# Kernel optimization log

Hardware: AMD Instinct MI355X
Metric: run time of the kernel (lower is better)

## Reference

```python
import jax, jax.numpy as jnp
import numpy as np

N_NODES = 50000
N_EDGES = 640000
IN_FEATS = 128
OUT_FEATS = 64
K = 2  # number of sparse sum-aggregation hops


def setup_inputs() -> dict:
    key = jax.random.key(0)
    k1, k2, k3, k4, k5 = jax.random.split(key, 5)
    features = jax.random.normal(k1, (N_NODES, IN_FEATS), dtype=jnp.float32)
    src = jax.random.randint(k2, (N_EDGES,), 0, N_NODES, dtype=jnp.int64)
    dst = jax.random.randint(k3, (N_EDGES,), 0, N_NODES, dtype=jnp.int64)
    weight = jax.random.normal(k4, (IN_FEATS, OUT_FEATS), dtype=jnp.float32) * (IN_FEATS ** -0.5)
    bias = jax.random.normal(k5, (OUT_FEATS,), dtype=jnp.float32) * 0.02
    return {"features": features, "src": src, "dst": dst, "weight": weight, "bias": bias}


def reference(features, src, dst, weight, bias):
    N = features.shape[0]
    ones = jnp.ones(src.shape[0], dtype=features.dtype)
    # degrees (graph is static across hops)
    out_deg = jax.ops.segment_sum(ones, src, num_segments=N)  # out-degree of each node
    in_deg = jax.ops.segment_sum(ones, dst, num_segments=N)   # in-degree of each node
    norm_src = jax.lax.rsqrt(jnp.clip(out_deg, 1.0))[:, None]
    norm_dst = jax.lax.rsqrt(jnp.clip(in_deg, 1.0))[:, None]

    # K hops of unnormalized copy_u/sum message passing
    h = features
    for _ in range(K):
        h = jax.ops.segment_sum(h[src], dst, num_segments=N)

    # GraphConv with norm='both': D_in^{-1/2} A^T D_out^{-1/2} h W + b
    h = h * norm_src
    h = h @ weight  # in_feats > out_feats: project before aggregating
    h = jax.ops.segment_sum(h[src], dst, num_segments=N)
    h = h * norm_dst + bias
    return h
```

## Files before the change

kernel.cpp:

```cpp
#include <hip/hip_runtime.h>
#include <hip/hip_bf16.h>

#define IN_FEATS 128
#define OUT_FEATS 64
#define HB_D 128
#define HB_S 64
#define PB 256
#define MAX_WORDS 12544
#define SMEM_U32 12544
#define PROJ_NODES 256

static inline char* align_up(char* p, size_t a) {
    return (char*)(((uintptr_t)p + a - 1) & ~(uintptr_t)(a - 1));
}

__device__ __forceinline__ unsigned pack_bf16(float a, float b) {
    unsigned ua = __float_as_uint(a), ub = __float_as_uint(b);
    ua = (ua + 0x7fffu + ((ua >> 16) & 1u)) >> 16;
    ub = (ub + 0x7fffu + ((ub >> 16) & 1u)) >> 16;
    return ua | (ub << 16);
}
__device__ __forceinline__ float bf16_lo(unsigned u) { return __uint_as_float(u << 16); }
__device__ __forceinline__ float bf16_hi(unsigned u) { return __uint_as_float(u & 0xffff0000u); }

__global__ __launch_bounds__(1024)
void hist_kernel(const int* __restrict__ src, const int* __restrict__ dst,
                 unsigned* __restrict__ partial, int* __restrict__ gcounter,
                 int E, int slice_d, int slice_s, int words) {
    __shared__ unsigned h[SMEM_U32];
    int tid = (int)threadIdx.x;
    int b = (int)blockIdx.x;

    if (b == 0 && tid == 0) *gcounter = 0;

    for (int w = tid; w < words; w += 1024) h[w] = 0u;
    __syncthreads();
    const int* __restrict__ keys;
    int sb, se;
    if (b < HB_D) { keys = dst; sb = b * slice_d; se = min(sb + slice_d, E); }
    else          { keys = src; sb = (b - HB_D) * slice_s; se = min(sb + slice_s, E); }
    for (int i = sb + tid * 4; i < se; i += 1024 * 4) {
        if (i + 3 < se) {
            int4 k4 = *reinterpret_cast<const int4*>(keys + i);
            atomicAdd(&h[k4.x >> 2], 1u << ((k4.x & 3) * 8));
            atomicAdd(&h[k4.y >> 2], 1u << ((k4.y & 3) * 8));
            atomicAdd(&h[k4.z >> 2], 1u << ((k4.z & 3) * 8));
            atomicAdd(&h[k4.w >> 2], 1u << ((k4.w & 3) * 8));
        } else {
            for (int j = i; j < se; ++j) {
                int k = keys[j];
                atomicAdd(&h[k >> 2], 1u << ((k & 3) * 8));
            }
        }
    }
    __syncthreads();
    unsigned* __restrict__ outp = partial + (size_t)b * words;
    for (int w = tid; w < words; w += 1024) outp[w] = h[w];
}

__global__ __launch_bounds__(PB)
void prefix_alloc_kernel(const unsigned* __restrict__ partial, unsigned* __restrict__ pprefix,
                         int2* __restrict__ rowext, float* __restrict__ normS,
                         float* __restrict__ normD, int* __restrict__ gcounter,
                         int N, int words) {
    __shared__ int tsum[PB];
    __shared__ int s_base;
    int tid = (int)threadIdx.x;
    int w = (int)blockIdx.x * PB + tid;
    unsigned run = 0, ssum = 0;
    if (w < words) {
        for (int bb = 0; bb < HB_D; bb += 16) {
            unsigned v[16], pfx[16];
#pragma unroll
            for (int i = 0; i < 16; ++i) v[i] = partial[(size_t)(bb + i) * words + w];
#pragma unroll
            for (int i = 0; i < 16; ++i) { pfx[i] = run; run += v[i]; }
#pragma unroll
            for (int i = 0; i < 16; ++i) pprefix[(size_t)(bb + i) * words + w] = pfx[i];
        }
        for (int bb = HB_D; bb < HB_D + HB_S; bb += 16) {
            unsigned v[16];
#pragma unroll
            for (int i = 0; i < 16; ++i) v[i] = partial[(size_t)(bb + i) * words + w];
#pragma unroll
            for (int i = 0; i < 16; ++i) ssum += v[i];
        }
    }
    int c0 = (int)(run & 0xffu), c1 = (int)((run >> 8) & 0xffu);
    int c2 = (int)((run >> 16) & 0xffu), c3 = (int)(run >> 24);
    int dtot = c0 + c1 + c2 + c3;
    tsum[tid] = dtot;
    __syncthreads();
    for (int off = 1; off < PB; off <<= 1) {
        int t = (tid >= off) ? tsum[tid - off] : 0;
        __syncthreads();
        tsum[tid] += t;
        __syncthreads();
    }
    if (tid == PB - 1) s_base = atomicAdd(gcounter, tsum[PB - 1]);
    __syncthreads();
    if (w < words) {
        int excl = tsum[tid] - dtot + s_base;
        int r0 = excl, r1 = r0 + c0, r2 = r1 + c1, r3 = r2 + c2;
        int base = 4 * w;
        if (base + 3 < N) {
            int4* re = reinterpret_cast<int4*>(rowext + base);
            re[0] = make_int4(r0, r1, r1, r2);
            re[1] = make_int4(r2, r3, r3, r3 + c3);
            float4 nD = make_float4(rsqrtf(fmaxf((float)c0, 1.f)), rsqrtf(fmaxf((float)c1, 1.f)),
                                    rsqrtf(fmaxf((float)c2, 1.f)), rsqrtf(fmaxf((float)c3, 1.f)));
            int s0 = (int)(ssum & 0xffu), s1 = (int)((ssum >> 8) & 0xffu);
            int s2 = (int)((ssum >> 16) & 0xffu), s3 = (int)(ssum >> 24);
            float4 nS = make_float4(rsqrtf(fmaxf((float)s0, 1.f)), rsqrtf(fmaxf((float)s1, 1.f)),
                                    rsqrtf(fmaxf((float)s2, 1.f)), rsqrtf(fmaxf((float)s3, 1.f)));
            *reinterpret_cast<float4*>(normD + base) = nD;
            *reinterpret_cast<float4*>(normS + base) = nS;
        } else {
            int r[5] = {r0, r1, r2, r3, r3 + c3};
            int cD[4] = {c0, c1, c2, c3};
            int cS[4] = {(int)(ssum & 0xffu), (int)((ssum >> 8) & 0xffu),
                         (int)((ssum >> 16) & 0xffu), (int)(ssum >> 24)};
            for (int i = 0; i < 4 && base + i < N; ++i) {
                rowext[base + i] = make_int2(r[i], r[i + 1]);
                normD[base + i] = rsqrtf(fmaxf((float)cD[i], 1.f));
                normS[base + i] = rsqrtf(fmaxf((float)cS[i], 1.f));
            }
        }
    }
}

__global__ __launch_bounds__(1024)
void fill_proj_kernel(const int* __restrict__ src, const int* __restrict__ dst,
                      const unsigned* __restrict__ pprefix, const int2* __restrict__ rowext,
                      unsigned short* __restrict__ csr16,
                      const float* __restrict__ X, const float* __restrict__ W,
                      uint2* __restrict__ Y,
                      int N, int E, int slice_d, int words) {
    __shared__ unsigned smem[SMEM_U32];
    int tid = (int)threadIdx.x;
    int b = (int)blockIdx.x;

    if (b < HB_D) {
        const unsigned* __restrict__ pp = pprefix + (size_t)b * words;
        for (int w = tid; w < words; w += 1024) smem[w] = pp[w];
        __syncthreads();
        int sb = b * slice_d;
        int se = min(sb + slice_d, E);
        for (int i = sb + tid * 4; i < se; i += 1024 * 4) {
            if (i + 3 < se) {
                int4 d4 = *reinterpret_cast<const int4*>(dst + i);
                int4 s4 = *reinterpret_cast<const int4*>(src + i);
                int dd[4] = {d4.x, d4.y, d4.z, d4.w};
                int ss[4] = {s4.x, s4.y, s4.z, s4.w};
#pragma unroll
                for (int j = 0; j < 4; ++j) {
                    int bin = dd[j];
                    unsigned sh = (unsigned)(bin & 3) * 8u;
                    unsigned old = atomicAdd(&smem[bin >> 2], 1u << sh);
                    int off = (int)((old >> sh) & 0xffu);
                    csr16[rowext[bin].x + off] = (unsigned short)ss[j];
                }
            } else {
                for (int j = i; j < se; ++j) {
                    int bin = dst[j];
                    unsigned sh = (unsigned)(bin & 3) * 8u;
                    unsigned old = atomicAdd(&smem[bin >> 2], 1u << sh);
                    int off = (int)((old >> sh) & 0xffu);
                    csr16[rowext[bin].x + off] = (unsigned short)src[j];
                }
            }
        }
    } else {
        float* w_s = (float*)smem;
        for (int i = tid; i < IN_FEATS * OUT_FEATS / 4; i += 1024)
            reinterpret_cast<float4*>(w_s)[i] = reinterpret_cast<const float4*>(W)[i];
        __syncthreads();
        int slot = tid >> 4;
        int jj = (tid & 15) * 4;
        int n0 = (b - HB_D) * PROJ_NODES + slot * 4;
        int m0 = min(n0 + 0, N - 1), m1 = min(n0 + 1, N - 1);
        int m2 = min(n0 + 2, N - 1), m3 = min(n0 + 3, N - 1);
        const float* __restrict__ x0p = X + (size_t)m0 * IN_FEATS;
        const float* __restrict__ x1p = X + (size_t)m1 * IN_FEATS;
        const float* __restrict__ x2p = X + (size_t)m2 * IN_FEATS;
        const float* __restrict__ x3p = X + (size_t)m3 * IN_FEATS;
        float4 a0 = make_float4(0.f, 0.f, 0.f, 0.f), a1 = a0, a2 = a0, a3 = a0;
#pragma unroll 2
        for (int k = 0; k < IN_FEATS; k += 4) {
            float4 x0 = *reinterpret_cast<const float4*>(x0p + k);
            float4 x1 = *reinterpret_cast<const float4*>(x1p + k);
            float4 x2 = *reinterpret_cast<const float4*>(x2p + k);
            float4 x3 = *reinterpret_cast<const float4*>(x3p + k);
#pragma unroll
            for (int q = 0; q < 4; ++q) {
                float4 w = *reinterpret_cast<const float4*>(&w_s[(k + q) * OUT_FEATS + jj]);
                float e0 = (q == 0) ? x0.x : (q == 1) ? x0.y : (q == 2) ? x0.z : x0.w;
                float e1 = (q == 0) ? x1.x : (q == 1) ? x1.y : (q == 2) ? x1.z : x1.w;
                float e2 = (q == 0) ? x2.x : (q == 1) ? x2.y : (q == 2) ? x2.z : x2.w;
                float e3 = (q == 0) ? x3.x : (q == 1) ? x3.y : (q == 2) ? x3.z : x3.w;
                a0.x = fmaf(e0, w.x, a0.x); a0.y = fmaf(e0, w.y, a0.y);
                a0.z = fmaf(e0, w.z, a0.z); a0.w = fmaf(e0, w.w, a0.w);
                a1.x = fmaf(e1, w.x, a1.x); a1.y = fmaf(e1, w.y, a1.y);
                a1.z = fmaf(e1, w.z, a1.z); a1.w = fmaf(e1, w.w, a1.w);
                a2.x = fmaf(e2, w.x, a2.x); a2.y = fmaf(e2, w.y, a2.y);
                a2.z = fmaf(e2, w.z, a2.z); a2.w = fmaf(e2, w.w, a2.w);
                a3.x = fmaf(e3, w.x, a3.x); a3.y = fmaf(e3, w.y, a3.y);
                a3.z = fmaf(e3, w.z, a3.z); a3.w = fmaf(e3, w.w, a3.w);
            }
        }
        float4 accs[4] = {a0, a1, a2, a3};
#pragma unroll
        for (int i = 0; i < 4; ++i) {
            int node = n0 + i;
            if (node < N) {
                uint2 o;
                o.x = pack_bf16(accs[i].x, accs[i].y);
                o.y = pack_bf16(accs[i].z, accs[i].w);
                Y[(size_t)node * (OUT_FEATS / 4) + (jj >> 2)] = o;
            }
        }
    }
}

template <int EPI>
__global__ __launch_bounds__(256)
void gather_hop(const uint4* __restrict__ Yin, const int2* __restrict__ rowext,
                const unsigned short* __restrict__ csr16, void* __restrict__ Yout,
                const float* __restrict__ vec, const float* __restrict__ bias,
                int N) {
    int g = ((int)threadIdx.x >> 3) & 7;
    int ci = (int)threadIdx.x & 7;
    int wid = (int)blockIdx.x * 4 + ((int)threadIdx.x >> 6);
    int nwaves = (int)gridDim.x * 4;
    for (int n0 = wid * 8; n0 < N; n0 += nwaves * 8) {
        int node = n0 + g;
        int beg = 0, end = 0;
        if (node < N) {
            int2 be = rowext[node];
            beg = be.x; end = be.y;
        }
        float4 aA = make_float4(0.f, 0.f, 0.f, 0.f), aB = aA;
        float4 bA = aA, bB = aA;
        int k = beg;
        for (; k + 1 < end; k += 2) {
            int s0 = (int)csr16[k];
            int s1 = (int)csr16[k + 1];
            uint4 v0 = Yin[(size_t)s0 * 8 + ci];
            uint4 v1 = Yin[(size_t)s1 * 8 + ci];
            aA.x += bf16_lo(v0.x); aA.y += bf16_hi(v0.x);
            aA.z += bf16_lo(v0.y); aA.w += bf16_hi(v0.y);
            aB.x += bf16_lo(v0.z); aB.y += bf16_hi(v0.z);
            aB.z += bf16_lo(v0.w); aB.w += bf16_hi(v0.w);
            bA.x += bf16_lo(v1.x); bA.y += bf16_hi(v1.x);
            bA.z += bf16_lo(v1.y); bA.w += bf16_hi(v1.y);
            bB.x += bf16_lo(v1.z); bB.y += bf16_hi(v1.z);
            bB.z += bf16_lo(v1.w); bB.w += bf16_hi(v1.w);
        }
        if (k < end) {
            uint4 v = Yin[(size_t)csr16[k] * 8 + ci];
            aA.x += bf16_lo(v.x); aA.y += bf16_hi(v.x);
            aA.z += bf16_lo(v.y); aA.w += bf16_hi(v.y);
            aB.x += bf16_lo(v.z); aB.y += bf16_hi(v.z);
            aB.z += bf16_lo(v.w); aB.w += bf16_hi(v.w);
        }
        if (node < N) {
            aA.x += bA.x; aA.y += bA.y; aA.z += bA.z; aA.w += bA.w;
            aB.x += bB.x; aB.y += bB.y; aB.z += bB.z; aB.w += bB.w;
            if (EPI == 1) {
                float sc = vec[node];
                aA.x *= sc; aA.y *= sc; aA.z *= sc; aA.w *= sc;
                aB.x *= sc; aB.y *= sc; aB.z *= sc; aB.w *= sc;
            }
            if (EPI == 2) {
                float sc = vec[node];
                float4 b0 = *reinterpret_cast<const float4*>(bias + ci * 8);
                float4 b1 = *reinterpret_cast<const float4*>(bias + ci * 8 + 4);
                aA.x = fmaf(aA.x, sc, b0.x); aA.y = fmaf(aA.y, sc, b0.y);
                aA.z = fmaf(aA.z, sc, b0.z); aA.w = fmaf(aA.w, sc, b0.w);
                aB.x = fmaf(aB.x, sc, b1.x); aB.y = fmaf(aB.y, sc, b1.y);
                aB.z = fmaf(aB.z, sc, b1.w == b1.w ? b1.z : b1.z); aB.w = fmaf(aB.w, sc, b1.w);
                float* op = (float*)Yout + (size_t)node * OUT_FEATS + ci * 8;
                *reinterpret_cast<float4*>(op) = aA;
                *reinterpret_cast<float4*>(op + 4) = aB;
            } else {
                uint4 o;
                o.x = pack_bf16(aA.x, aA.y);
                o.y = pack_bf16(aA.z, aA.w);
                o.z = pack_bf16(aB.x, aB.y);
                o.w = pack_bf16(aB.z, aB.w);
                reinterpret_cast<uint4*>(Yout)[(size_t)node * 8 + ci] = o;
            }
        }
    }
}

extern "C" void kernel_launch(void* const* d_in, const int* in_sizes, int n_in,
                              void* d_out, int out_size, void* d_ws, size_t ws_size,
                              hipStream_t stream) {
    const float* features = (const float*)d_in[0];
    const int*   src      = (const int*)d_in[1];
    const int*   dst      = (const int*)d_in[2];
    const float* weight   = (const float*)d_in[3];
    const float* bias     = (const float*)d_in[4];

    const int N = in_sizes[0] / IN_FEATS;
    const int E = in_sizes[1];
    const int words = (N + 3) / 4;
    const int NB = (words + PB - 1) / PB;
    const int slice_d = (((E + HB_D - 1) / HB_D) + 3) & ~3;
    const int slice_s = (((E + HB_S - 1) / HB_S) + 3) & ~3;
    const int projBlocks = (N + PROJ_NODES - 1) / PROJ_NODES;

    char* p = (char*)d_ws;
    float* normS   = (float*)p;  p = align_up(p + sizeof(float) * (N + 4), 256);
    float* normD   = (float*)p;  p = align_up(p + sizeof(float) * (N + 4), 256);
    uint2* y0      = (uint2*)p;  p = align_up(p + sizeof(uint2) * (size_t)N * (OUT_FEATS / 4), 256);
    uint2* y1      = (uint2*)p;  p = align_up(p + sizeof(uint2) * (size_t)N * (OUT_FEATS / 4), 256);
    int2*  rowext  = (int2*)p;   p = align_up(p + sizeof(int2) * (N + 4), 256);
    int*   gcounter= (int*)p;    p = align_up(p + sizeof(int) * 4, 256);
    unsigned short* csr16 = (unsigned short*)p;  p = align_up(p + sizeof(unsigned short) * (size_t)E, 256);
    unsigned* partial = (unsigned*)p;  p = align_up(p + sizeof(unsigned) * (size_t)(HB_D + HB_S) * words, 256);
    unsigned* pprefix = (unsigned*)p;  p = align_up(p + sizeof(unsigned) * (size_t)HB_D * words, 256);

    float* out = (float*)d_out;

    hist_kernel<<<HB_D + HB_S, 1024, 0, stream>>>(
        src, dst, partial, gcounter, E, slice_d, slice_s, words);
    prefix_alloc_kernel<<<NB, PB, 0, stream>>>(partial, pprefix, rowext, normS, normD,
                                               gcounter, N, words);
    fill_proj_kernel<<<HB_D + projBlocks, 1024, 0, stream>>>(
        src, dst, pprefix, rowext, csr16, features, weight, y0, N, E, slice_d, words);

    const int hop_blocks = (N + 31) / 32;
    gather_hop<0><<<hop_blocks, 256, 0, stream>>>((const uint4*)y0, rowext, csr16, (void*)y1, nullptr, nullptr, N);
    gather_hop<1><<<hop_blocks, 256, 0, stream>>>((const uint4*)y1, rowext, csr16, (void*)y0, normS, nullptr, N);
    gather_hop<2><<<hop_blocks, 256, 0, stream>>>((const uint4*)y0, rowext, csr16, (void*)out, normD, bias, N);
}
```

Measured before the change: 91.93 us.

## Fuse prefix-alloc into fill/projection kernel with cross-block flag handoff

Merges the prefix/allocation kernel into the CSR fill plus projection kernel. The first 13 blocks compute the prefix, row extents and norms, then signal a global release counter. Fill blocks spin on that counter with an acquire load before scattering, while projection blocks run independently and overlap the prefix work. This removes one kernel launch and its serialization. It relies on the prefix blocks being scheduled before or alongside the spinning fill blocks, and they have the lowest block indices. It also cleans up a no-op bias expression.

```diff
diff --git a/kernel.cpp b/kernel.cpp
--- a/kernel.cpp
+++ b/kernel.cpp
@@ -5,7 +5,9 @@
 #define OUT_FEATS 64
 #define HB_D 128
 #define HB_S 64
-#define PB 256
+#define PREF_BLOCKS 13
+#define FILL_BASE PREF_BLOCKS
+#define PROJ_BASE (PREF_BLOCKS + HB_D)
 #define MAX_WORDS 12544
 #define SMEM_U32 12544
 #define PROJ_NODES 256
@@ -25,13 +27,13 @@
 
 __global__ __launch_bounds__(1024)
 void hist_kernel(const int* __restrict__ src, const int* __restrict__ dst,
-                 unsigned* __restrict__ partial, int* __restrict__ gcounter,
+                 unsigned* __restrict__ partial, int* __restrict__ flags,
                  int E, int slice_d, int slice_s, int words) {
     __shared__ unsigned h[SMEM_U32];
     int tid = (int)threadIdx.x;
     int b = (int)blockIdx.x;
 
-    if (b == 0 && tid == 0) *gcounter = 0;
+    if (b == 0 && tid < 32) flags[tid] = 0;
 
     for (int w = tid; w < words; w += 1024) h[w] = 0u;
     __syncthreads();
@@ -58,93 +60,101 @@
     for (int w = tid; w < words; w += 1024) outp[w] = h[w];
 }
 
-__global__ __launch_bounds__(PB)
-void prefix_alloc_kernel(const unsigned* __restrict__ partial, unsigned* __restrict__ pprefix,
-                         int2* __restrict__ rowext, float* __restrict__ normS,
-                         float* __restrict__ normD, int* __restrict__ gcounter,
-                         int N, int words) {
-    __shared__ int tsum[PB];
+__global__ __launch_bounds__(1024)
+void build_kernel(const int* __restrict__ src, const int* __restrict__ dst,
+                  const unsigned* __restrict__ partial, unsigned* __restrict__ pprefix,
+                  int2* __restrict__ rowext, float* __restrict__ normS,
+                  float* __restrict__ normD, unsigned short* __restrict__ csr16,
+                  const float* __restrict__ X, const float* __restrict__ W,
+                  uint2* __restrict__ Y, int* __restrict__ flags,
+                  int N, int E, int slice_d, int words) {
+    __shared__ unsigned smem[SMEM_U32];
     __shared__ int s_base;
     int tid = (int)threadIdx.x;
-    int w = (int)blockIdx.x * PB + tid;
-    unsigned run = 0, ssum = 0;
-    if (w < words) {
-        for (int bb = 0; bb < HB_D; bb += 16) {
-            unsigned v[16], pfx[16];
-#pragma unroll
-            for (int i = 0; i < 16; ++i) v[i] = partial[(size_t)(bb + i) * words + w];
-#pragma unroll
-            for (int i = 0; i < 16; ++i) { pfx[i] = run; run += v[i]; }
-#pragma unroll
-            for (int i = 0; i < 16; ++i) pprefix[(size_t)(bb + i) * words + w] = pfx[i];
-        }
-        for (int bb = HB_D; bb < HB_D + HB_S; bb += 16) {
-            unsigned v[16];
-#pragma unroll
-            for (int i = 0; i < 16; ++i) v[i] = partial[(size_t)(bb + i) * words + w];
-#pragma unroll
-            for (int i = 0; i < 16; ++i) ssum += v[i];
-        }
-    }
-    int c0 = (int)(run & 0xffu), c1 = (int)((run >> 8) & 0xffu);
-    int c2 = (int)((run >> 16) & 0xffu), c3 = (int)(run >> 24);
-    int dtot = c0 + c1 + c2 + c3;
-    tsum[tid] = dtot;
-    __syncthreads();
-    for (int off = 1; off < PB; off <<= 1) {
-        int t = (tid >= off) ? tsum[tid - off] : 0;
-        __syncthreads();
-        tsum[tid] += t;
-        __syncthreads();
-    }
-    if (tid == PB - 1) s_base = atomicAdd(gcounter, tsum[PB - 1]);
-    __syncthreads();
-    if (w < words) {
-        int excl = tsum[tid] - dtot + s_base;
-        int r0 = excl, r1 = r0 + c0, r2 = r1 + c1, r3 = r2 + c2;
-        int base = 4 * w;
-        if (base + 3 < N) {
-            int4* re = reinterpret_cast<int4*>(rowext + base);
-            re[0] = make_int4(r0, r1, r1, r2);
-            re[1] = make_int4(r2, r3, r3, r3 + c3);
-            float4 nD = make_float4(rsqrtf(fmaxf((float)c0, 1.f)), rsqrtf(fmaxf((float)c1, 1.f)),
-                                    rsqrtf(fmaxf((float)c2, 1.f)), rsqrtf(fmaxf((float)c3, 1.f)));
-            int s0 = (int)(ssum & 0xffu), s1 = (int)((ssum >> 8) & 0xffu);
-            int s2 = (int)((ssum >> 16) & 0xffu), s3 = (int)(ssum >> 24);
-            float4 nS = make_float4(rsqrtf(fmaxf((float)s0, 1.f)), rsqrtf(fmaxf((float)s1, 1.f)),
-                                    rsqrtf(fmaxf((float)s2, 1.f)), rsqrtf(fmaxf((float)s3, 1.f)));
-            *reinterpret_cast<float4*>(normD + base) = nD;
-            *reinterpret_cast<float4*>(normS + base) = nS;
-        } else {
-            int r[5] = {r0, r1, r2, r3, r3 + c3};
-            int cD[4] = {c0, c1, c2, c3};
-            int cS[4] = {(int)(ssum & 0xffu), (int)((ssum >> 8) & 0xffu),
-                         (int)((ssum >> 16) & 0xffu), (int)(ssum >> 24)};
-            for (int i = 0; i < 4 && base + i < N; ++i) {
-                rowext[base + i] = make_int2(r[i], r[i + 1]);
-                normD[base + i] = rsqrtf(fmaxf((float)cD[i], 1.f));
-                normS[base + i] = rsqrtf(fmaxf((float)cS[i], 1.f));
-            }
-        }
-    }
-}
-
-__global__ __launch_bounds__(1024)
-void fill_proj_kernel(const int* __restrict__ src, const int* __restrict__ dst,
-                      const unsigned* __restrict__ pprefix, const int2* __restrict__ rowext,
-                      unsigned short* __restrict__ csr16,
-                      const float* __restrict__ X, const float* __restrict__ W,
-                      uint2* __restrict__ Y,
-                      int N, int E, int slice_d, int words) {
-    __shared__ unsigned smem[SMEM_U32];
-    int tid = (int)threadIdx.x;
     int b = (int)blockIdx.x;
 
-    if (b < HB_D) {
-        const unsigned* __restrict__ pp = pprefix + (size_t)b * words;
+    if (b < PREF_BLOCKS) {
+        int w = b * 1024 + tid;
+        unsigned run = 0, ssum = 0;
+        if (w < words) {
+            for (int bb = 0; bb < HB_D; bb += 16) {
+                unsigned v[16], pfx[16];
+#pragma unroll
+                for (int i = 0; i < 16; ++i) v[i] = partial[(size_t)(bb + i) * words + w];
+#pragma unroll
+                for (int i = 0; i < 16; ++i) { pfx[i] = run; run += v[i]; }
+#pragma unroll
+                for (int i = 0; i < 16; ++i) pprefix[(size_t)(bb + i) * words + w] = pfx[i];
+            }
+            for (int bb = HB_D; bb < HB_D + HB_S; bb += 16) {
+                unsigned v[16];
+#pragma unroll
+                for (int i = 0; i < 16; ++i) v[i] = partial[(size_t)(bb + i) * words + w];
+#pragma unroll
+                for (int i = 0; i < 16; ++i) ssum += v[i];
+            }
+        }
+        int c0 = (int)(run & 0xffu), c1 = (int)((run >> 8) & 0xffu);
+        int c2 = (int)((run >> 16) & 0xffu), c3 = (int)(run >> 24);
+        int dtot = c0 + c1 + c2 + c3;
+        int* tsum = (int*)smem;
+        tsum[tid] = dtot;
+        __syncthreads();
+        for (int off = 1; off < 1024; off <<= 1) {
+            int t = (tid >= off) ? tsum[tid - off] : 0;
+            __syncthreads();
+            tsum[tid] += t;
+            __syncthreads();
+        }
+        if (tid == 1023)
+            s_base = __hip_atomic_fetch_add(&flags[16], tsum[1023],
+                                            __ATOMIC_RELAXED, __HIP_MEMORY_SCOPE_AGENT);
+        __syncthreads();
+        if (w < words) {
+            int excl = tsum[tid] - dtot + s_base;
+            int r0 = excl, r1 = r0 + c0, r2 = r1 + c1, r3 = r2 + c2;
+            int base = 4 * w;
+            if (base + 3 < N) {
+                int4* re = reinterpret_cast<int4*>(rowext + base);
+                re[0] = make_int4(r0, r1, r1, r2);
+                re[1] = make_int4(r2, r3, r3, r3 + c3);
+                float4 nD = make_float4(rsqrtf(fmaxf((float)c0, 1.f)), rsqrtf(fmaxf((float)c1, 1.f)),
+                                        rsqrtf(fmaxf((float)c2, 1.f)), rsqrtf(fmaxf((float)c3, 1.f)));
+                int s0 = (int)(ssum & 0xffu), s1 = (int)((ssum >> 8) & 0xffu);
+                int s2 = (int)((ssum >> 16) & 0xffu), s3 = (int)(ssum >> 24);
+                float4 nS = make_float4(rsqrtf(fmaxf((float)s0, 1.f)), rsqrtf(fmaxf((float)s1, 1.f)),
+                                        rsqrtf(fmaxf((float)s2, 1.f)), rsqrtf(fmaxf((float)s3, 1.f)));
+                *reinterpret_cast<float4*>(normD + base) = nD;
+                *reinterpret_cast<float4*>(normS + base) = nS;
+            } else {
+                int r[5] = {r0, r1, r2, r3, r3 + c3};
+                int cD[4] = {c0, c1, c2, c3};
+                int cS[4] = {(int)(ssum & 0xffu), (int)((ssum >> 8) & 0xffu),
+                             (int)((ssum >> 16) & 0xffu), (int)(ssum >> 24)};
+                for (int i = 0; i < 4 && base + i < N; ++i) {
+                    rowext[base + i] = make_int2(r[i], r[i + 1]);
+                    normD[base + i] = rsqrtf(fmaxf((float)cD[i], 1.f));
+                    normS[base + i] = rsqrtf(fmaxf((float)cS[i], 1.f));
+                }
+            }
+        }
+        __syncthreads();
+        if (tid == 0) {
+            __threadfence();
+            __hip_atomic_fetch_add(&flags[0], 1, __ATOMIC_RELEASE, __HIP_MEMORY_SCOPE_AGENT);
+        }
+    } else if (b < PROJ_BASE) {
+        int fb = b - FILL_BASE;
+        if (tid == 0) {
+            while (__hip_atomic_load(&flags[0], __ATOMIC_ACQUIRE, __HIP_MEMORY_SCOPE_AGENT)
+                   < PREF_BLOCKS)
+                __builtin_amdgcn_s_sleep(16);
+        }
+        __syncthreads();
+        const unsigned* __restrict__ pp = pprefix + (size_t)fb * words;
         for (int w = tid; w < words; w += 1024) smem[w] = pp[w];
         __syncthreads();
-        int sb = b * slice_d;
+        int sb = fb * slice_d;
         int se = min(sb + slice_d, E);
         for (int i = sb + tid * 4; i < se; i += 1024 * 4) {
             if (i + 3 < se) {
@@ -177,7 +187,7 @@
         __syncthreads();
         int slot = tid >> 4;
         int jj = (tid & 15) * 4;
-        int n0 = (b - HB_D) * PROJ_NODES + slot * 4;
+        int n0 = (b - PROJ_BASE) * PROJ_NODES + slot * 4;
         int m0 = min(n0 + 0, N - 1), m1 = min(n0 + 1, N - 1);
         int m2 = min(n0 + 2, N - 1), m3 = min(n0 + 3, N - 1);
         const float* __restrict__ x0p = X + (size_t)m0 * IN_FEATS;
@@ -278,7 +288,7 @@
                 aA.x = fmaf(aA.x, sc, b0.x); aA.y = fmaf(aA.y, sc, b0.y);
                 aA.z = fmaf(aA.z, sc, b0.z); aA.w = fmaf(aA.w, sc, b0.w);
                 aB.x = fmaf(aB.x, sc, b1.x); aB.y = fmaf(aB.y, sc, b1.y);
-                aB.z = fmaf(aB.z, sc, b1.w == b1.w ? b1.z : b1.z); aB.w = fmaf(aB.w, sc, b1.w);
+                aB.z = fmaf(aB.z, sc, b1.z); aB.w = fmaf(aB.w, sc, b1.w);
                 float* op = (float*)Yout + (size_t)node * OUT_FEATS + ci * 8;
                 *reinterpret_cast<float4*>(op) = aA;
                 *reinterpret_cast<float4*>(op + 4) = aB;
@@ -306,7 +316,6 @@
     const int N = in_sizes[0] / IN_FEATS;
     const int E = in_sizes[1];
     const int words = (N + 3) / 4;
-    const int NB = (words + PB - 1) / PB;
     const int slice_d = (((E + HB_D - 1) / HB_D) + 3) & ~3;
     const int slice_s = (((E + HB_S - 1) / HB_S) + 3) & ~3;
     const int projBlocks = (N + PROJ_NODES - 1) / PROJ_NODES;
@@ -317,7 +326,7 @@
     uint2* y0      = (uint2*)p;  p = align_up(p + sizeof(uint2) * (size_t)N * (OUT_FEATS / 4), 256);
     uint2* y1      = (uint2*)p;  p = align_up(p + sizeof(uint2) * (size_t)N * (OUT_FEATS / 4), 256);
     int2*  rowext  = (int2*)p;   p = align_up(p + sizeof(int2) * (N + 4), 256);
-    int*   gcounter= (int*)p;    p = align_up(p + sizeof(int) * 4, 256);
+    int*   flags   = (int*)p;    p = align_up(p + sizeof(int) * 32, 256);
     unsigned short* csr16 = (unsigned short*)p;  p = align_up(p + sizeof(unsigned short) * (size_t)E, 256);
     unsigned* partial = (unsigned*)p;  p = align_up(p + sizeof(unsigned) * (size_t)(HB_D + HB_S) * words, 256);
     unsigned* pprefix = (unsigned*)p;  p = align_up(p + sizeof(unsigned) * (size_t)HB_D * words, 256);
@@ -325,11 +334,10 @@
     float* out = (float*)d_out;
 
     hist_kernel<<<HB_D + HB_S, 1024, 0, stream>>>(
-        src, dst, partial, gcounter, E, slice_d, slice_s, words);
-    prefix_alloc_kernel<<<NB, PB, 0, stream>>>(partial, pprefix, rowext, normS, normD,
-                                               gcounter, N, words);
-    fill_proj_kernel<<<HB_D + projBlocks, 1024, 0, stream>>>(
-        src, dst, pprefix, rowext, csr16, features, weight, y0, N, E, slice_d, words);
+        src, dst, partial, flags, E, slice_d, slice_s, words);
+    build_kernel<<<PROJ_BASE + projBlocks, 1024, 0, stream>>>(
+        src, dst, partial, pprefix, rowext, normS, normD, csr16,
+        features, weight, y0, flags, N, E, slice_d, words);
 
     const int hop_blocks = (N + 31) / 32;
     gather_hop<0><<<hop_blocks, 256, 0, stream>>>((const uint4*)y0, rowext, csr16, (void*)y1, nullptr, nullptr, N);
```

New measurement: 143.0 us. 55.5% more time.
